# Performance work log

Measured on AMD Instinct MI355X. Metric: run time of the kernel, lower is better.

## Reference

```python
import jax, jax.numpy as jnp
import numpy as np

EMBED_DIM = 512
NUM_HEADS = 8
HEAD_DIM = EMBED_DIM // NUM_HEADS
SCALE = HEAD_DIM ** -0.5
TEMP = 1.0


def setup_inputs() -> dict:
    key = jax.random.key(0)
    ks = jax.random.split(key, 12)
    B, N, Nk, C = 4, 2048, 2048, EMBED_DIM
    s = C ** -0.5
    return {
        "x": jax.random.normal(ks[0], (B, N, C), jnp.float32),
        "y": jax.random.normal(ks[1], (B, Nk, C), jnp.float32),
        "z": jax.random.normal(ks[2], (B, Nk, C), jnp.float32),
        "Wq": jax.random.normal(ks[3], (C, C), jnp.float32) * s,
        "bq": jnp.zeros((C,), jnp.float32),
        "Wk": jax.random.normal(ks[4], (C, C), jnp.float32) * s,
        "bk": jnp.zeros((C,), jnp.float32),
        "Wv": jax.random.normal(ks[5], (C, C), jnp.float32) * s,
        "bv": jnp.zeros((C,), jnp.float32),
        "Wo": jax.random.normal(ks[6], (C, C), jnp.float32) * s,
        "bo": jnp.zeros((C,), jnp.float32),
    }


def reference(x, y, z, Wq, bq, Wk, bk, Wv, bv, Wo, bo):
    B, N, C = x.shape
    Nk = y.shape[1]
    H, D = NUM_HEADS, HEAD_DIM

    def split_heads(t, L):
        return t.reshape(B, L, H, D).transpose(0, 2, 1, 3)  # [B,H,L,D]

    q = split_heads(x @ Wq.T + bq, N)
    k = split_heads(y @ Wk.T + bk, Nk)
    v = split_heads(z @ Wv.T + bv, Nk)

    # [B,H,N,Nk] logits, scaled
    logits = jnp.einsum("bhnd,bhkd->bhnk", q, k) * SCALE

    # Gumbel-softmax (soft, tau=TEMP) with a fixed noise key
    gkey = jax.random.key(42)
    gumbels = jax.random.gumbel(gkey, logits.shape, logits.dtype)
    attn = jax.nn.softmax((logits + gumbels) / TEMP, axis=-1)

    out = jnp.einsum("bhnk,bhkd->bhnd", attn, v)
    out = out.transpose(0, 2, 1, 3).reshape(B, N, C)
    return out @ Wo.T + bo
```

## Files before the change

kernel.cpp:

```cpp
#include <hip/hip_runtime.h>
#include <hip/hip_bf16.h>
#include <stdint.h>

#define Bdim 4
#define Hdim 8
#define Ndim 2048
#define Cdim 512
#define Ddim 64
#define SCALE_F 0.125f
#define SOFTMAX_SHIFT 30.0f

typedef __bf16 bf16_t;
typedef __bf16 bf16x8 __attribute__((ext_vector_type(8)));
typedef float f32x4 __attribute__((ext_vector_type(4)));

#define SWZ_XOR_F(v, m) \
  __int_as_float(__builtin_amdgcn_ds_swizzle(__float_as_int(v), (0x1F | ((m) << 10))))

__device__ __forceinline__ float gumbel_noise(uint32_t flat) {
  const uint32_t k0 = 0u, k1 = 42u, k2 = 0x1BD11BDAu ^ 0u ^ 42u;
  uint32_t x0 = 0u;
  uint32_t x1 = flat;
  x0 += k0; x1 += k1;
#define TF_R(r) { x0 += x1; x1 = __builtin_rotateleft32(x1, r); x1 ^= x0; }
#define TF_R4A TF_R(13) TF_R(15) TF_R(26) TF_R(6)
#define TF_R4B TF_R(17) TF_R(29) TF_R(16) TF_R(24)
  TF_R4A  x0 += k1; x1 += k2 + 1u;
  TF_R4B  x0 += k2; x1 += k0 + 2u;
  TF_R4A  x0 += k0; x1 += k1 + 3u;
  TF_R4B  x0 += k1; x1 += k2 + 4u;
  TF_R4A  x0 += k2; x1 += k0 + 5u;
#undef TF_R4B
#undef TF_R4A
#undef TF_R
  uint32_t bits = x0 ^ x1;
  float f = __uint_as_float((bits >> 9) | 0x3F800000u) - 1.0f;
  float u = f + 1.17549435e-38f;
  return -__logf(-__logf(u));
}

__global__ void cvt_f32_bf16(const float* __restrict__ in,
                             bf16_t* __restrict__ out, int n8) {
  int i = blockIdx.x * blockDim.x + threadIdx.x;
  if (i < n8) {
    const float4* p = (const float4*)in + (size_t)i * 2;
    float4 a = p[0], b = p[1];
    union { bf16_t h[8]; uint4 u; } pk;
    pk.h[0] = (bf16_t)a.x; pk.h[1] = (bf16_t)a.y;
    pk.h[2] = (bf16_t)a.z; pk.h[3] = (bf16_t)a.w;
    pk.h[4] = (bf16_t)b.x; pk.h[5] = (bf16_t)b.y;
    pk.h[6] = (bf16_t)b.z; pk.h[7] = (bf16_t)b.w;
    *((uint4*)out + i) = pk.u;
  }
}

__device__ __forceinline__ void gemm_core(const bf16_t* __restrict__ A,
                                          const bf16_t* __restrict__ W,
                                          int m0, int n0,
                                          bf16_t* As, bf16_t* Ws,
                                          f32x4 (&acc)[4][4]) {
  const int t = threadIdx.x;
  const int wave = t >> 6, lane = t & 63;
  const int ln = lane & 15, qd = lane >> 4;
  const int wm = wave >> 1, wn = wave & 1;

#pragma unroll
  for (int i = 0; i < 4; i++)
#pragma unroll
    for (int j = 0; j < 4; j++) acc[i][j] = (f32x4){0.f, 0.f, 0.f, 0.f};

  for (int kt = 0; kt < Cdim / 64; ++kt) {
#pragma unroll
    for (int it = 0; it < 4; ++it) {
      int vec = it * 256 + t;
      int row = vec >> 3, c8 = (vec & 7) * 8;
      *(bf16x8*)&As[row * 72 + c8] =
          *(const bf16x8*)&A[(size_t)(m0 + row) * Cdim + kt * 64 + c8];
      *(bf16x8*)&Ws[row * 72 + c8] =
          *(const bf16x8*)&W[(size_t)(n0 + row) * Cdim + kt * 64 + c8];
    }
    __syncthreads();
#pragma unroll
    for (int ks = 0; ks < 2; ++ks) {
      bf16x8 af[4], bfr[4];
#pragma unroll
      for (int i = 0; i < 4; i++)
        af[i] = *(const bf16x8*)&As[(wm * 64 + i * 16 + ln) * 72 + ks * 32 + qd * 8];
#pragma unroll
      for (int j = 0; j < 4; j++)
        bfr[j] = *(const bf16x8*)&Ws[(wn * 64 + j * 16 + ln) * 72 + ks * 32 + qd * 8];
#pragma unroll
      for (int i = 0; i < 4; i++)
#pragma unroll
        for (int j = 0; j < 4; j++)
          acc[i][j] = __builtin_amdgcn_mfma_f32_16x16x32_bf16(af[i], bfr[j],
                                                              acc[i][j], 0, 0, 0);
    }
    __syncthreads();
  }
}

__global__ __launch_bounds__(256, 2)
void qkv_gemm_kernel(const bf16_t* __restrict__ xb, const bf16_t* __restrict__ yb,
                     const bf16_t* __restrict__ zb, const bf16_t* __restrict__ wqb,
                     const bf16_t* __restrict__ wkb, const bf16_t* __restrict__ wvb,
                     const float* __restrict__ bq, const float* __restrict__ bk,
                     const float* __restrict__ bv, bf16_t* __restrict__ qo,
                     bf16_t* __restrict__ ko, bf16_t* __restrict__ vo) {
  __shared__ bf16_t As[128 * 72];
  __shared__ bf16_t Ws[128 * 72];
  const int sel = blockIdx.z;
  const bf16_t* A = sel == 0 ? xb : (sel == 1 ? yb : zb);
  const bf16_t* W = sel == 0 ? wqb : (sel == 1 ? wkb : wvb);
  const float* bias = sel == 0 ? bq : (sel == 1 ? bk : bv);
  bf16_t* O = sel == 0 ? qo : (sel == 1 ? ko : vo);
  const float mul = sel == 0 ? SCALE_F : 1.0f;
  const int m0 = blockIdx.y * 128, n0 = blockIdx.x * 128;

  f32x4 acc[4][4];
  gemm_core(A, W, m0, n0, As, Ws, acc);

  const int t = threadIdx.x;
  const int wave = t >> 6, lane = t & 63;
  const int ln = lane & 15, qd = lane >> 4;
  const int wm = wave >> 1, wn = wave & 1;
#pragma unroll
  for (int i = 0; i < 4; i++)
#pragma unroll
    for (int j = 0; j < 4; j++)
#pragma unroll
      for (int r = 0; r < 4; r++) {
        int grow = m0 + wm * 64 + i * 16 + qd * 4 + r;
        int gcol = n0 + wn * 64 + j * 16 + ln;
        float val = (acc[i][j][r] + bias[gcol]) * mul;
        int b = grow >> 11, n = grow & 2047;
        int h = gcol >> 6, d = gcol & 63;
        O[(((size_t)b * Hdim + h) * Ndim + n) * Ddim + d] = (bf16_t)val;
      }
}

__global__ __launch_bounds__(256, 2)
void out_gemm_kernel(const bf16_t* __restrict__ ab, const bf16_t* __restrict__ wob,
                     const float* __restrict__ bo, float* __restrict__ out) {
  __shared__ bf16_t As[128 * 72];
  __shared__ bf16_t Ws[128 * 72];
  const int m0 = blockIdx.y * 128, n0 = blockIdx.x * 128;
  f32x4 acc[4][4];
  gemm_core(ab, wob, m0, n0, As, Ws, acc);

  const int t = threadIdx.x;
  const int wave = t >> 6, lane = t & 63;
  const int ln = lane & 15, qd = lane >> 4;
  const int wm = wave >> 1, wn = wave & 1;
#pragma unroll
  for (int i = 0; i < 4; i++)
#pragma unroll
    for (int j = 0; j < 4; j++)
#pragma unroll
      for (int r = 0; r < 4; r++) {
        int grow = m0 + wm * 64 + i * 16 + qd * 4 + r;
        int gcol = n0 + wn * 64 + j * 16 + ln;
        out[(size_t)grow * Cdim + gcol] = acc[i][j][r] + bo[gcol];
      }
}

__global__ __launch_bounds__(256, 4)
void attn_kernel(const bf16_t* __restrict__ qb, const bf16_t* __restrict__ kb,
                 const bf16_t* __restrict__ vb, bf16_t* __restrict__ ab) {
  __shared__ bf16_t Ks[64 * 72];
  __shared__ bf16_t Vt[64 * 72];
  __shared__ bf16_t Ps[64 * 72];

  const int t = threadIdx.x;
  const int wave = t >> 6, lane = t & 63;
  const int ln = lane & 15, qd = lane >> 4;
  const int qtile = blockIdx.x;
  const int bh = blockIdx.y;
  const int qbase = qtile * 64;

  const bf16_t* Qg = qb + (size_t)bh * Ndim * Ddim;
  const bf16_t* Kg = kb + (size_t)bh * Ndim * Ddim;
  const bf16_t* Vg = vb + (size_t)bh * Ndim * Ddim;

  const bf16_t* Qrow = Qg + (size_t)(qbase + wave * 16 + ln) * Ddim;
  bf16x8 qf0 = *(const bf16x8*)&Qrow[qd * 8];
  bf16x8 qf1 = *(const bf16x8*)&Qrow[32 + qd * 8];

  float l_r[4] = {0.f, 0.f, 0.f, 0.f};
  f32x4 o_acc[4];
#pragma unroll
  for (int j = 0; j < 4; j++) o_acc[j] = (f32x4){0.f, 0.f, 0.f, 0.f};

  const uint32_t flat_bh = (uint32_t)bh << 22;

  for (int kt = 0; kt < Ndim / 64; ++kt) {
#pragma unroll
    for (int it = 0; it < 2; ++it) {
      int vec = it * 256 + t;
      int row = vec >> 3, c8 = (vec & 7) * 8;
      *(bf16x8*)&Ks[row * 72 + c8] =
          *(const bf16x8*)&Kg[(size_t)(kt * 64 + row) * Ddim + c8];
      bf16x8 vv = *(const bf16x8*)&Vg[(size_t)(kt * 64 + row) * Ddim + c8];
      int swz_base = ((row >> 3) ^ (c8 >> 3)) * 8 + (row & 7);
#pragma unroll
      for (int jj = 0; jj < 8; jj++)
        Vt[(c8 + jj) * 72 + swz_base] = vv[jj];
    }
    __syncthreads();

    f32x4 s[4];
#pragma unroll
    for (int j = 0; j < 4; j++) s[j] = (f32x4){0.f, 0.f, 0.f, 0.f};
#pragma unroll
    for (int j = 0; j < 4; j++) {
      bf16x8 bk0 = *(const bf16x8*)&Ks[(j * 16 + ln) * 72 + qd * 8];
      bf16x8 bk1 = *(const bf16x8*)&Ks[(j * 16 + ln) * 72 + 32 + qd * 8];
      s[j] = __builtin_amdgcn_mfma_f32_16x16x32_bf16(qf0, bk0, s[j], 0, 0, 0);
      s[j] = __builtin_amdgcn_mfma_f32_16x16x32_bf16(qf1, bk1, s[j], 0, 0, 0);
    }

#pragma unroll
    for (int r = 0; r < 4; r++) {
      int qrow = qbase + wave * 16 + qd * 4 + r;
      uint32_t fbase = flat_bh + ((uint32_t)qrow << 11) + (uint32_t)(kt * 64 + ln);
#pragma unroll
      for (int j = 0; j < 4; j++) {
        float sv = s[j][r] + gumbel_noise(fbase + j * 16) - SOFTMAX_SHIFT;
        float pv = __expf(sv);
        l_r[r] += pv;
        Ps[(wave * 16 + qd * 4 + r) * 72 + j * 16 + ln] = (bf16_t)pv;
      }
    }

#pragma unroll
    for (int ks = 0; ks < 2; ++ks) {
      bf16x8 af = *(const bf16x8*)&Ps[(wave * 16 + ln) * 72 + ks * 32 + qd * 8];
#pragma unroll
      for (int j = 0; j < 4; j++) {
        int d = j * 16 + ln;
        bf16x8 bv8 = *(const bf16x8*)&Vt[d * 72 + (((ks * 4 + qd) ^ (d >> 3)) << 3)];
        o_acc[j] = __builtin_amdgcn_mfma_f32_16x16x32_bf16(af, bv8, o_acc[j], 0, 0, 0);
      }
    }
    __syncthreads();
  }

  float linv[4];
#pragma unroll
  for (int r = 0; r < 4; r++) {
    float lsum = l_r[r];
    lsum += SWZ_XOR_F(lsum, 1);
    lsum += SWZ_XOR_F(lsum, 2);
    lsum += SWZ_XOR_F(lsum, 4);
    lsum += SWZ_XOR_F(lsum, 8);
    linv[r] = __frcp_rn(lsum);
  }
  const int b = bh >> 3, h = bh & 7;
#pragma unroll
  for (int j = 0; j < 4; j++)
#pragma unroll
    for (int r = 0; r < 4; r++) {
      int qrow = qbase + wave * 16 + qd * 4 + r;
      int col = h * 64 + j * 16 + ln;
      ab[((size_t)b * Ndim + qrow) * Cdim + col] = (bf16_t)(o_acc[j][r] * linv[r]);
    }
}

extern "C" void kernel_launch(void* const* d_in, const int* in_sizes, int n_in,
                              void* d_out, int out_size, void* d_ws, size_t ws_size,
                              hipStream_t stream) {
  const float* x  = (const float*)d_in[0];
  const float* y  = (const float*)d_in[1];
  const float* z  = (const float*)d_in[2];
  const float* Wq = (const float*)d_in[3];
  const float* bq = (const float*)d_in[4];
  const float* Wk = (const float*)d_in[5];
  const float* bk = (const float*)d_in[6];
  const float* Wv = (const float*)d_in[7];
  const float* bv = (const float*)d_in[8];
  const float* Wo = (const float*)d_in[9];
  const float* bo = (const float*)d_in[10];
  float* out = (float*)d_out;

  bf16_t* base = (bf16_t*)d_ws;
  const size_t NBIG = (size_t)Bdim * Ndim * Cdim;
  const size_t NW   = (size_t)Cdim * Cdim;
  bf16_t* xb  = base;
  bf16_t* yb  = xb + NBIG;
  bf16_t* zb  = yb + NBIG;
  bf16_t* wqb = zb + NBIG;
  bf16_t* wkb = wqb + NW;
  bf16_t* wvb = wkb + NW;
  bf16_t* wob = wvb + NW;
  bf16_t* qb  = wob + NW;
  bf16_t* kb  = qb + NBIG;
  bf16_t* vb  = kb + NBIG;
  bf16_t* ab  = vb + NBIG;

  int n8b = (int)(NBIG / 8), n8w = (int)(NW / 8);
  cvt_f32_bf16<<<n8b / 256, 256, 0, stream>>>(x, xb, n8b);
  cvt_f32_bf16<<<n8b / 256, 256, 0, stream>>>(y, yb, n8b);
  cvt_f32_bf16<<<n8b / 256, 256, 0, stream>>>(z, zb, n8b);
  cvt_f32_bf16<<<n8w / 256, 256, 0, stream>>>(Wq, wqb, n8w);
  cvt_f32_bf16<<<n8w / 256, 256, 0, stream>>>(Wk, wkb, n8w);
  cvt_f32_bf16<<<n8w / 256, 256, 0, stream>>>(Wv, wvb, n8w);
  cvt_f32_bf16<<<n8w / 256, 256, 0, stream>>>(Wo, wob, n8w);

  qkv_gemm_kernel<<<dim3(Cdim / 128, (Bdim * Ndim) / 128, 3), 256, 0, stream>>>(
      xb, yb, zb, wqb, wkb, wvb, bq, bk, bv, qb, kb, vb);

  attn_kernel<<<dim3(Ndim / 64, Bdim * Hdim), 256, 0, stream>>>(qb, kb, vb, ab);

  out_gemm_kernel<<<dim3(Cdim / 128, (Bdim * Ndim) / 128), 256, 0, stream>>>(
      ab, wob, bo, out);
}
```

Measured before the change: 512.0 us.

## Split attention key range across two blocks and combine partials

The attention kernel now splits the key dimension in two via a third grid dimension. Each half writes unnormalized fp32 partial outputs and row sums to workspace, and a new combine kernel sums the halves, normalizes, and writes the bf16 output. This doubles the attention grid from 1024 to 2048 blocks to improve occupancy across the MI355X compute units. The cost is extra fp32 partial traffic and one more kernel launch. A fixed softmax shift instead of a running max makes the two partials directly additive.

```diff
diff --git a/kernel.cpp b/kernel.cpp
--- a/kernel.cpp
+++ b/kernel.cpp
@@ -9,6 +9,7 @@
 #define Ddim 64
 #define SCALE_F 0.125f
 #define SOFTMAX_SHIFT 30.0f
+#define KSPLIT 2
 
 typedef __bf16 bf16_t;
 typedef __bf16 bf16x8 __attribute__((ext_vector_type(8)));
@@ -166,7 +167,8 @@
 
 __global__ __launch_bounds__(256, 4)
 void attn_kernel(const bf16_t* __restrict__ qb, const bf16_t* __restrict__ kb,
-                 const bf16_t* __restrict__ vb, bf16_t* __restrict__ ab) {
+                 const bf16_t* __restrict__ vb, float* __restrict__ part_o,
+                 float* __restrict__ part_l) {
   __shared__ bf16_t Ks[64 * 72];
   __shared__ bf16_t Vt[64 * 72];
   __shared__ bf16_t Ps[64 * 72];
@@ -176,7 +178,10 @@
   const int ln = lane & 15, qd = lane >> 4;
   const int qtile = blockIdx.x;
   const int bh = blockIdx.y;
+  const int z = blockIdx.z;
   const int qbase = qtile * 64;
+  const int kt_lo = z * (Ndim / 64 / KSPLIT);
+  const int kt_hi = kt_lo + (Ndim / 64 / KSPLIT);
 
   const bf16_t* Qg = qb + (size_t)bh * Ndim * Ddim;
   const bf16_t* Kg = kb + (size_t)bh * Ndim * Ddim;
@@ -193,7 +198,7 @@
 
   const uint32_t flat_bh = (uint32_t)bh << 22;
 
-  for (int kt = 0; kt < Ndim / 64; ++kt) {
+  for (int kt = kt_lo; kt < kt_hi; ++kt) {
 #pragma unroll
     for (int it = 0; it < 2; ++it) {
       int vec = it * 256 + t;
@@ -245,7 +250,10 @@
     __syncthreads();
   }
 
-  float linv[4];
+  const int pidx = ((bh << 5) | qtile) * KSPLIT + z;
+  float* po = part_o + (size_t)pidx * 64 * 64;
+  float* pl = part_l + (size_t)pidx * 64;
+
 #pragma unroll
   for (int r = 0; r < 4; r++) {
     float lsum = l_r[r];
@@ -253,17 +261,45 @@
     lsum += SWZ_XOR_F(lsum, 2);
     lsum += SWZ_XOR_F(lsum, 4);
     lsum += SWZ_XOR_F(lsum, 8);
-    linv[r] = __frcp_rn(lsum);
-  }
+    if (ln == 0) pl[wave * 16 + qd * 4 + r] = lsum;
+  }
+#pragma unroll
+  for (int j = 0; j < 4; j++)
+#pragma unroll
+    for (int r = 0; r < 4; r++) {
+      int row = wave * 16 + qd * 4 + r;
+      int col = j * 16 + ln;
+      po[row * 64 + col] = o_acc[j][r];
+    }
+}
+
+__global__ __launch_bounds__(256, 8)
+void attn_combine(const float* __restrict__ part_o,
+                  const float* __restrict__ part_l, bf16_t* __restrict__ ab) {
+  const int blk = blockIdx.x;
+  const int bh = blk >> 5, qtile = blk & 31;
+  const float* o0 = part_o + (size_t)(blk * KSPLIT + 0) * 64 * 64;
+  const float* o1 = part_o + (size_t)(blk * KSPLIT + 1) * 64 * 64;
+  const float* l0 = part_l + (size_t)(blk * KSPLIT + 0) * 64;
+  const float* l1 = part_l + (size_t)(blk * KSPLIT + 1) * 64;
+
+  const int t = threadIdx.x;
+  const int row = t >> 2, c0 = (t & 3) * 16;
+  const float linv = 1.0f / (l0[row] + l1[row]);
   const int b = bh >> 3, h = bh & 7;
-#pragma unroll
-  for (int j = 0; j < 4; j++)
-#pragma unroll
-    for (int r = 0; r < 4; r++) {
-      int qrow = qbase + wave * 16 + qd * 4 + r;
-      int col = h * 64 + j * 16 + ln;
-      ab[((size_t)b * Ndim + qrow) * Cdim + col] = (bf16_t)(o_acc[j][r] * linv[r]);
-    }
+  bf16_t* dst = ab + ((size_t)b * Ndim + qtile * 64 + row) * Cdim + h * 64 + c0;
+
+#pragma unroll
+  for (int i = 0; i < 4; i++) {
+    float4 a = *(const float4*)&o0[row * 64 + c0 + i * 4];
+    float4 c = *(const float4*)&o1[row * 64 + c0 + i * 4];
+    union { bf16_t h4[4]; uint2 u; } pk;
+    pk.h4[0] = (bf16_t)((a.x + c.x) * linv);
+    pk.h4[1] = (bf16_t)((a.y + c.y) * linv);
+    pk.h4[2] = (bf16_t)((a.z + c.z) * linv);
+    pk.h4[3] = (bf16_t)((a.w + c.w) * linv);
+    *(uint2*)&dst[i * 4] = pk.u;
+  }
 }
 
 extern "C" void kernel_launch(void* const* d_in, const int* in_sizes, int n_in,
@@ -296,6 +332,8 @@
   bf16_t* kb  = qb + NBIG;
   bf16_t* vb  = kb + NBIG;
   bf16_t* ab  = vb + NBIG;
+  float* part_o = (float*)(ab + NBIG);
+  float* part_l = part_o + (size_t)1024 * KSPLIT * 64 * 64;
 
   int n8b = (int)(NBIG / 8), n8w = (int)(NW / 8);
   cvt_f32_bf16<<<n8b / 256, 256, 0, stream>>>(x, xb, n8b);
@@ -309,7 +347,10 @@
   qkv_gemm_kernel<<<dim3(Cdim / 128, (Bdim * Ndim) / 128, 3), 256, 0, stream>>>(
       xb, yb, zb, wqb, wkb, wvb, bq, bk, bv, qb, kb, vb);
 
-  attn_kernel<<<dim3(Ndim / 64, Bdim * Hdim), 256, 0, stream>>>(qb, kb, vb, ab);
+  attn_kernel<<<dim3(Ndim / 64, Bdim * Hdim, KSPLIT), 256, 0, stream>>>(
+      qb, kb, vb, part_o, part_l);
+
+  attn_combine<<<dim3(1024), 256, 0, stream>>>(part_o, part_l, ab);
 
   out_gemm_kernel<<<dim3(Cdim / 128, (Bdim * Ndim) / 128), 256, 0, stream>>>(
       ab, wob, bo, out);
```

After: 494.2 us. -3.5%, faster.
